# Kernel tuning notes

Hardware: AMD Instinct MI355X
Metric: run time of the kernel (lower is better)

Reference implementation:

```python
import jax, jax.numpy as jnp
import numpy as np

B, L, D = 2, 2048, 1024
H = 16
HD = D // H  # 64


def setup_inputs() -> dict:
    key = jax.random.key(0)
    k1, k2, k3, k4 = jax.random.split(key, 4)
    s = 0.02
    x = jax.random.normal(k1, (B, L, D), dtype=jnp.float32)
    qkv_w = jax.random.normal(k2, (3 * D, D), dtype=jnp.float32) * s
    out_w = jax.random.normal(k3, (D, D), dtype=jnp.float32) * s
    out_b = jax.random.normal(k4, (D,), dtype=jnp.float32) * s
    return {"x": x, "qkv_w": qkv_w, "out_w": out_w, "out_b": out_b}


def reference(x, qkv_w, out_w, out_b):
    b, l, d = x.shape
    # qkv projection (no bias): [B,L,3D] -> [3,B,H,L,HD]
    qkv = jnp.einsum('bld,ed->ble', x, qkv_w)
    qkv = qkv.reshape(b, l, 3, H, HD).transpose(2, 0, 3, 1, 4)
    q, k, v = qkv[0], qkv[1], qkv[2]
    # scaled dot-product scores [B,H,L,L]
    scores = jnp.einsum('bhqd,bhkd->bhqk', q, k) / jnp.sqrt(jnp.float32(HD))
    causal_mask = jnp.triu(jnp.ones((l, l), dtype=bool), k=1)
    scores = jnp.where(causal_mask, -jnp.inf, scores)
    probs = jax.nn.softmax(scores, axis=-1)
    # dropout is identity in eval / p=0
    out = jnp.einsum('bhqk,bhkd->bhqd', probs, v)
    out = out.transpose(0, 2, 1, 3).reshape(b, l, d)
    return out @ out_w.T + out_b
```

## Files before the change

kernel.cpp:

```cpp
#include <hip/hip_runtime.h>
#include <hip/hip_bf16.h>
#include <cstdint>


typedef __attribute__((ext_vector_type(8))) short sh8;
typedef __attribute__((ext_vector_type(4))) short sh4;
typedef __attribute__((ext_vector_type(4))) float f32x4;

__device__ __forceinline__ unsigned short f2b(float f) {
  unsigned int u = __float_as_uint(f);
  u += 0x7FFFu + ((u >> 16) & 1u);
  return (unsigned short)(u >> 16);
}

__device__ __forceinline__ unsigned int pack2(float lo, float hi) {
  return (unsigned int)f2b(lo) | ((unsigned int)f2b(hi) << 16);
}

__device__ __forceinline__ f32x4 mfma16x16x16(sh4 a, sh4 b, f32x4 c) {
#if __has_builtin(__builtin_amdgcn_mfma_f32_16x16x16bf16_1k)
  return __builtin_amdgcn_mfma_f32_16x16x16bf16_1k(a, b, c, 0, 0, 0);
#else
  asm volatile("v_mfma_f32_16x16x16_bf16 %0, %1, %2, %0" : "+v"(c) : "v"(a), "v"(b));
  return c;
#endif
}

__device__ __forceinline__ void gload_lds16(const void* g, void* l) {
  __builtin_amdgcn_global_load_lds((__attribute__((address_space(1))) void*)g,
                                   (__attribute__((address_space(3))) void*)l,
                                   16, 0, 0);
}

__global__ __launch_bounds__(256) void k_cvt(const float* __restrict__ in,
                                             unsigned short* __restrict__ out, int n) {
  int idx = (blockIdx.x * 256 + threadIdx.x) * 4;
  if (idx >= n) return;
  float4 v = *(const float4*)&in[idx];
  union { unsigned short u[4]; uint2 w; } r;
  r.u[0] = f2b(v.x); r.u[1] = f2b(v.y); r.u[2] = f2b(v.z); r.u[3] = f2b(v.w);
  *(uint2*)&out[idx] = r.w;
}

template<int MT, int NT>
__device__ __forceinline__ void gemm_bt_core(
    const unsigned short* __restrict__ A,
    const unsigned short* __restrict__ B,
    int K, int m0, int n0,
    unsigned short* ldsA, unsigned short* ldsB,
    f32x4 acc[MT][NT]) {
  constexpr int TA = MT;
  constexpr int TB = NT;
  const int tid  = threadIdx.x;
  const int wv   = tid >> 6;
  const int lane = tid & 63;
  const int wm = (wv >> 1) * (MT * 16);
  const int wn = (wv & 1) * (NT * 16);
  const int fr = lane & 15;
  const int g  = lane >> 4;

  for (int k0 = 0; k0 < K; k0 += 64) {
#pragma unroll
    for (int t = 0; t < TA; ++t) {
      int gi = t * 256 + tid;
      int r = gi >> 3, c = gi & 7;
      gload_lds16(&A[(size_t)(m0 + r) * K + k0 + ((c ^ (r & 7)) << 3)], &ldsA[gi * 8]);
    }
#pragma unroll
    for (int t = 0; t < TB; ++t) {
      int gi = t * 256 + tid;
      int r = gi >> 3, c = gi & 7;
      gload_lds16(&B[(size_t)(n0 + r) * K + k0 + ((c ^ (r & 7)) << 3)], &ldsB[gi * 8]);
    }
    __syncthreads();
#pragma unroll
    for (int ks = 0; ks < 2; ++ks) {
      sh8 af[MT], bf[NT];
#pragma unroll
      for (int mt = 0; mt < MT; ++mt)
        af[mt] = *(const sh8*)&ldsA[(wm + mt * 16 + fr) * 64 +
                                    ((((ks << 2) + g) ^ (fr & 7)) << 3)];
#pragma unroll
      for (int nt = 0; nt < NT; ++nt)
        bf[nt] = *(const sh8*)&ldsB[(wn + nt * 16 + fr) * 64 +
                                    ((((ks << 2) + g) ^ (fr & 7)) << 3)];
#pragma unroll
      for (int mt = 0; mt < MT; ++mt)
#pragma unroll
        for (int nt = 0; nt < NT; ++nt)
          acc[mt][nt] = __builtin_amdgcn_mfma_f32_16x16x32_bf16(af[mt], bf[nt], acc[mt][nt], 0, 0, 0);
    }
    __syncthreads();
  }
}

__global__ __launch_bounds__(256, 5) void k_qkv_gemm(
    const unsigned short* __restrict__ xb, const unsigned short* __restrict__ wq,
    unsigned short* __restrict__ Q, unsigned short* __restrict__ Kc,
    unsigned short* __restrict__ Vt) {
  __shared__ __align__(16) unsigned short ldsA[64 * 64];
  __shared__ __align__(16) unsigned short ldsB[128 * 64];
  f32x4 acc[2][4];
  const f32x4 fz = {0.f, 0.f, 0.f, 0.f};
#pragma unroll
  for (int i = 0; i < 2; ++i)
#pragma unroll
    for (int j = 0; j < 4; ++j) acc[i][j] = fz;

  const int m0 = blockIdx.x * 64, n0 = blockIdx.y * 128;
  gemm_bt_core<2, 4>(xb, wq, 1024, m0, n0, ldsA, ldsB, acc);

  const int tid = threadIdx.x, wv = tid >> 6, lane = tid & 63;
  const int wm = (wv >> 1) << 5, wn = (wv & 1) << 6;
  const int r4 = (lane >> 4) << 2, fr = lane & 15;
#pragma unroll
  for (int mt = 0; mt < 2; ++mt)
#pragma unroll
    for (int nt = 0; nt < 4; ++nt) {
      const int row0 = m0 + wm + mt * 16 + r4;
      const int col  = n0 + wn + nt * 16 + fr;
      const int b = row0 >> 11;
      const int which = col >> 10, rem = col & 1023;
      const int h = rem >> 6, hd = rem & 63;
      const size_t bh = (size_t)(b * 16 + h);
      if (which == 2) {
        const size_t vb = (bh * 64 + hd) * 2048 + (row0 & 2047);
        *(unsigned int*)&Vt[vb]     = pack2(acc[mt][nt][0], acc[mt][nt][1]);
        *(unsigned int*)&Vt[vb + 2] = pack2(acc[mt][nt][2], acc[mt][nt][3]);
      } else {
#pragma unroll
        for (int i = 0; i < 4; ++i) {
          const int lq = (row0 + i) & 2047;
          float v = acc[mt][nt][i];
          if (which == 0) Q [(bh * 2048 + lq) * 64 + hd] = f2b(v * 0.125f);
          else            Kc[(bh * 2048 + lq) * 64 + hd] = f2b(v);
        }
      }
    }
}

__global__ __launch_bounds__(256, 4) void k_attn(
    const unsigned short* __restrict__ Q, const unsigned short* __restrict__ Kc,
    const unsigned short* __restrict__ Vt, unsigned short* __restrict__ attn) {
  __shared__ __align__(16) unsigned short kbuf[2][64 * 64];
  __shared__ __align__(16) unsigned short vbuf[2][64 * 64];

  const int bh  = blockIdx.x & 31;
  const int grp = 31 - (blockIdx.x >> 5);
  const int wv = threadIdx.x >> 6, lane = threadIdx.x & 63;
  const int tid = threadIdx.x;
  const int strip = (grp << 2) + wv;
  const int qw = strip << 4;
  const int b = bh >> 4, h = bh & 15;
  const unsigned short* Qb = Q  + (size_t)bh * 2048 * 64;
  const unsigned short* Kb = Kc + (size_t)bh * 2048 * 64;
  const unsigned short* Vb = Vt + (size_t)bh * 64 * 2048;
  const int fr = lane & 15, g = lane >> 4;
  const int fk = g << 3, r4 = g << 2;
  const f32x4 fz = {0.f, 0.f, 0.f, 0.f};

  const int sgr0 = tid >> 3,        sgc0 = tid & 7;
  const int sgr1 = (tid + 256) >> 3, sgc1 = tid & 7;

  sh8 qf[2];
#pragma unroll
  for (int ks = 0; ks < 2; ++ks)
    qf[ks] = *(const sh8*)&Qb[(size_t)(qw + fr) * 64 + ks * 32 + fk];

  f32x4 o[4];
#pragma unroll
  for (int i = 0; i < 4; ++i) o[i] = fz;
  float m_i = -1e30f, lp = 0.f;

  const int njm = grp + 1;

  gload_lds16(&Kb[(size_t)sgr0 * 64 + ((sgc0 ^ (sgr0 & 7)) << 3)], &kbuf[0][tid * 8]);
  gload_lds16(&Kb[(size_t)sgr1 * 64 + ((sgc1 ^ (sgr1 & 7)) << 3)], &kbuf[0][(tid + 256) * 8]);
  gload_lds16(&Vb[(size_t)sgr0 * 2048 + ((sgc0 ^ (sgr0 & 7)) << 3)], &vbuf[0][tid * 8]);
  gload_lds16(&Vb[(size_t)sgr1 * 2048 + ((sgc1 ^ (sgr1 & 7)) << 3)], &vbuf[0][(tid + 256) * 8]);

  for (int j = 0; j < njm; ++j) {
    __syncthreads();
    if (j + 1 < njm) {
      const int kvn = (j + 1) << 6;
      const int nb = (j + 1) & 1;
      gload_lds16(&Kb[(size_t)(kvn + sgr0) * 64 + ((sgc0 ^ (sgr0 & 7)) << 3)], &kbuf[nb][tid * 8]);
      gload_lds16(&Kb[(size_t)(kvn + sgr1) * 64 + ((sgc1 ^ (sgr1 & 7)) << 3)], &kbuf[nb][(tid + 256) * 8]);
      gload_lds16(&Vb[(size_t)sgr0 * 2048 + kvn + ((sgc0 ^ (sgr0 & 7)) << 3)], &vbuf[nb][tid * 8]);
      gload_lds16(&Vb[(size_t)sgr1 * 2048 + kvn + ((sgc1 ^ (sgr1 & 7)) << 3)], &vbuf[nb][(tid + 256) * 8]);
    }
    const int kvb = j << 6;
    const unsigned short* kb = kbuf[j & 1];
    const unsigned short* vb = vbuf[j & 1];
    f32x4 s[4];
#pragma unroll
    for (int t = 0; t < 4; ++t) s[t] = fz;
#pragma unroll
    for (int ks = 0; ks < 2; ++ks)
#pragma unroll
      for (int t = 0; t < 4; ++t) {
        sh8 kf = *(const sh8*)&kb[(t * 16 + fr) * 64 + ((((ks << 2) + g) ^ (fr & 7)) << 3)];
        s[t] = __builtin_amdgcn_mfma_f32_16x16x32_bf16(kf, qf[ks], s[t], 0, 0, 0);
      }

    if (j == njm - 1) {
#pragma unroll
      for (int t = 0; t < 4; ++t)
#pragma unroll
        for (int i = 0; i < 4; ++i)
          if (kvb + t * 16 + r4 + i > qw + fr) s[t][i] = -1e30f;
    }
    float pm = s[0][0];
#pragma unroll
    for (int t = 0; t < 4; ++t)
#pragma unroll
      for (int i = 0; i < 4; ++i) pm = fmaxf(pm, s[t][i]);
    if (!__all(pm - m_i <= 8.0f)) {
      float rm = fmaxf(pm, __shfl_xor(pm, 16, 64));
      rm = fmaxf(rm, __shfl_xor(rm, 32, 64));
      const float mn = fmaxf(m_i, rm);
      const float sc = __expf(m_i - mn);
      m_i = mn;
      lp *= sc;
#pragma unroll
      for (int hb = 0; hb < 4; ++hb)
#pragma unroll
        for (int i = 0; i < 4; ++i) o[hb][i] *= sc;
    }
#pragma unroll
    for (int t = 0; t < 4; ++t) {
#pragma unroll
      for (int i = 0; i < 4; ++i) s[t][i] = __expf(s[t][i] - m_i);
      lp += (s[t][0] + s[t][1]) + (s[t][2] + s[t][3]);
    }
#pragma unroll
    for (int t = 0; t < 4; ++t) {
      union { unsigned int w[2]; sh4 v; } pb;
      pb.w[0] = pack2(s[t][0], s[t][1]);
      pb.w[1] = pack2(s[t][2], s[t][3]);
#pragma unroll
      for (int hb = 0; hb < 4; ++hb) {
        sh4 vf = *(const sh4*)&vb[(hb * 16 + fr) * 64 +
                                  ((((t << 1) + (g >> 1)) ^ (fr & 7)) << 3) + ((g & 1) << 2)];
        o[hb] = mfma16x16x16(vf, pb.v, o[hb]);
      }
    }
  }

  float l = lp;
  l += __shfl_xor(l, 16, 64);
  l += __shfl_xor(l, 32, 64);
  const float inv = 1.0f / l;
  const size_t base = ((size_t)(b * 2048 + qw + fr)) * 1024 + h * 64;
#pragma unroll
  for (int hb = 0; hb < 4; ++hb)
#pragma unroll
    for (int i2 = 0; i2 < 2; ++i2) {
      unsigned int pw = pack2(o[hb][2 * i2] * inv, o[hb][2 * i2 + 1] * inv);
      *(unsigned int*)&attn[base + hb * 16 + r4 + 2 * i2] = pw;
    }
}

__global__ __launch_bounds__(256, 5) void k_out_gemm(
    const unsigned short* __restrict__ attn, const unsigned short* __restrict__ wo,
    const float* __restrict__ bias, float* __restrict__ out) {
  __shared__ __align__(16) unsigned short ldsA[64 * 64];
  __shared__ __align__(16) unsigned short ldsB[64 * 64];
  f32x4 acc[2][2];
  const f32x4 fz = {0.f, 0.f, 0.f, 0.f};
#pragma unroll
  for (int i = 0; i < 2; ++i)
#pragma unroll
    for (int j = 0; j < 2; ++j) acc[i][j] = fz;

  const int m0 = blockIdx.x * 64, n0 = blockIdx.y * 64;
  gemm_bt_core<2, 2>(attn, wo, 1024, m0, n0, ldsA, ldsB, acc);

  const int tid = threadIdx.x, wv = tid >> 6, lane = tid & 63;
  const int wm = (wv >> 1) << 5, wn = (wv & 1) << 5;
  const int r4 = (lane >> 4) << 2, fr = lane & 15;
#pragma unroll
  for (int mt = 0; mt < 2; ++mt)
#pragma unroll
    for (int nt = 0; nt < 2; ++nt)
#pragma unroll
      for (int i = 0; i < 4; ++i) {
        int row = m0 + wm + mt * 16 + r4 + i;
        int col = n0 + wn + nt * 16 + fr;
        out[(size_t)row * 1024 + col] = acc[mt][nt][i] + bias[col];
      }
}

extern "C" void kernel_launch(void* const* d_in, const int* in_sizes, int n_in,
                              void* d_out, int out_size, void* d_ws, size_t ws_size,
                              hipStream_t stream) {
  const float* x     = (const float*)d_in[0];
  const float* qkv_w = (const float*)d_in[1];
  const float* out_w = (const float*)d_in[2];
  const float* out_b = (const float*)d_in[3];
  float* out = (float*)d_out;

  unsigned short* ws   = (unsigned short*)d_ws;
  unsigned short* xb   = ws;
  unsigned short* wq   = xb  + 4096 * 1024;
  unsigned short* wo   = wq  + 3072 * 1024;
  unsigned short* Qs   = wo  + 1024 * 1024;
  unsigned short* Ks   = Qs  + 32 * 2048 * 64;
  unsigned short* Vts  = Ks  + 32 * 2048 * 64;
  unsigned short* attn = Vts + 32 * 64 * 2048;

  k_cvt<<<4096, 256, 0, stream>>>(x,     xb, 4096 * 1024);
  k_cvt<<<3072, 256, 0, stream>>>(qkv_w, wq, 3072 * 1024);
  k_cvt<<<1024, 256, 0, stream>>>(out_w, wo, 1024 * 1024);
  k_qkv_gemm<<<dim3(64, 24), 256, 0, stream>>>(xb, wq, Qs, Ks, Vts);
  k_attn<<<1024, 256, 0, stream>>>(Qs, Ks, Vts, attn);
  k_out_gemm<<<dim3(64, 16), 256, 0, stream>>>(attn, wo, out_b, out);
}
```

Measured before the change: 106.5 us.

## Double-buffer LDS tiles in shared GEMM core to overlap loads with MFMA

The shared bf16 GEMM core now uses two LDS buffers. It issues the global-to-LDS load for the next K tile before computing on the current one, and drops one of the two barriers per iteration. The goal is to hide global load latency behind MFMA work in both the QKV and output projection GEMMs. This doubles the LDS footprint, and the QKV kernel's occupancy hint drops from 5 to 3 blocks per CU.

```diff
diff --git a/kernel.cpp b/kernel.cpp
--- a/kernel.cpp
+++ b/kernel.cpp
@@ -49,8 +49,8 @@
     int K, int m0, int n0,
     unsigned short* ldsA, unsigned short* ldsB,
     f32x4 acc[MT][NT]) {
-  constexpr int TA = MT;
-  constexpr int TB = NT;
+  constexpr int ASZ = MT * 32 * 64;
+  constexpr int BSZ = NT * 32 * 64;
   const int tid  = threadIdx.x;
   const int wv   = tid >> 6;
   const int lane = tid & 63;
@@ -59,47 +59,55 @@
   const int fr = lane & 15;
   const int g  = lane >> 4;
 
-  for (int k0 = 0; k0 < K; k0 += 64) {
-#pragma unroll
-    for (int t = 0; t < TA; ++t) {
+  auto stage = [&](int k0, unsigned short* dA, unsigned short* dB) {
+#pragma unroll
+    for (int t = 0; t < MT; ++t) {
       int gi = t * 256 + tid;
       int r = gi >> 3, c = gi & 7;
-      gload_lds16(&A[(size_t)(m0 + r) * K + k0 + ((c ^ (r & 7)) << 3)], &ldsA[gi * 8]);
-    }
-#pragma unroll
-    for (int t = 0; t < TB; ++t) {
+      gload_lds16(&A[(size_t)(m0 + r) * K + k0 + ((c ^ (r & 7)) << 3)], &dA[gi * 8]);
+    }
+#pragma unroll
+    for (int t = 0; t < NT; ++t) {
       int gi = t * 256 + tid;
       int r = gi >> 3, c = gi & 7;
-      gload_lds16(&B[(size_t)(n0 + r) * K + k0 + ((c ^ (r & 7)) << 3)], &ldsB[gi * 8]);
-    }
+      gload_lds16(&B[(size_t)(n0 + r) * K + k0 + ((c ^ (r & 7)) << 3)], &dB[gi * 8]);
+    }
+  };
+
+  const int nk = K >> 6;
+  stage(0, ldsA, ldsB);
+  for (int kk = 0; kk < nk; ++kk) {
     __syncthreads();
+    if (kk + 1 < nk)
+      stage((kk + 1) << 6, ldsA + ((kk + 1) & 1) * ASZ, ldsB + ((kk + 1) & 1) * BSZ);
+    const unsigned short* a = ldsA + (kk & 1) * ASZ;
+    const unsigned short* b = ldsB + (kk & 1) * BSZ;
 #pragma unroll
     for (int ks = 0; ks < 2; ++ks) {
       sh8 af[MT], bf[NT];
 #pragma unroll
       for (int mt = 0; mt < MT; ++mt)
-        af[mt] = *(const sh8*)&ldsA[(wm + mt * 16 + fr) * 64 +
-                                    ((((ks << 2) + g) ^ (fr & 7)) << 3)];
+        af[mt] = *(const sh8*)&a[(wm + mt * 16 + fr) * 64 +
+                                 ((((ks << 2) + g) ^ (fr & 7)) << 3)];
 #pragma unroll
       for (int nt = 0; nt < NT; ++nt)
-        bf[nt] = *(const sh8*)&ldsB[(wn + nt * 16 + fr) * 64 +
-                                    ((((ks << 2) + g) ^ (fr & 7)) << 3)];
+        bf[nt] = *(const sh8*)&b[(wn + nt * 16 + fr) * 64 +
+                                 ((((ks << 2) + g) ^ (fr & 7)) << 3)];
 #pragma unroll
       for (int mt = 0; mt < MT; ++mt)
 #pragma unroll
         for (int nt = 0; nt < NT; ++nt)
           acc[mt][nt] = __builtin_amdgcn_mfma_f32_16x16x32_bf16(af[mt], bf[nt], acc[mt][nt], 0, 0, 0);
     }
-    __syncthreads();
   }
 }
 
-__global__ __launch_bounds__(256, 5) void k_qkv_gemm(
+__global__ __launch_bounds__(256, 3) void k_qkv_gemm(
     const unsigned short* __restrict__ xb, const unsigned short* __restrict__ wq,
     unsigned short* __restrict__ Q, unsigned short* __restrict__ Kc,
     unsigned short* __restrict__ Vt) {
-  __shared__ __align__(16) unsigned short ldsA[64 * 64];
-  __shared__ __align__(16) unsigned short ldsB[128 * 64];
+  __shared__ __align__(16) unsigned short ldsA[2 * 64 * 64];
+  __shared__ __align__(16) unsigned short ldsB[2 * 128 * 64];
   f32x4 acc[2][4];
   const f32x4 fz = {0.f, 0.f, 0.f, 0.f};
 #pragma unroll
@@ -264,8 +272,8 @@
 __global__ __launch_bounds__(256, 5) void k_out_gemm(
     const unsigned short* __restrict__ attn, const unsigned short* __restrict__ wo,
     const float* __restrict__ bias, float* __restrict__ out) {
-  __shared__ __align__(16) unsigned short ldsA[64 * 64];
-  __shared__ __align__(16) unsigned short ldsB[64 * 64];
+  __shared__ __align__(16) unsigned short ldsA[2 * 64 * 64];
+  __shared__ __align__(16) unsigned short ldsB[2 * 64 * 64];
   f32x4 acc[2][2];
   const f32x4 fz = {0.f, 0.f, 0.f, 0.f};
 #pragma unroll
```

After: 106.5 us. No clear change (-0.0%).
